# Performance work log

Measured on AMD Instinct MI355X. Metric: run time of the kernel, lower is better.

Reference implementation:

```python
import jax, jax.numpy as jnp
import numpy as np

B, S, D, H = 4, 4096, 1024, 64

def setup_inputs() -> dict:
    key = jax.random.key(0)
    k1, k2, k3, k4 = jax.random.split(key, 4)
    x = jax.random.normal(k1, (B, S, D), dtype=jnp.float32)
    scale = D ** -0.5
    Wq = jax.random.normal(k2, (D, H), dtype=jnp.float32) * scale
    Wk = jax.random.normal(k3, (D, H), dtype=jnp.float32) * scale
    Wv = jax.random.normal(k4, (D, H), dtype=jnp.float32) * scale
    return {"x": x, "Wq": Wq, "Wk": Wk, "Wv": Wv}

def reference(x, Wq, Wk, Wv):
    # Projections: [B,S,D] @ [D,H] -> [B,S,H]
    Q = jnp.einsum('bsd,dh->bsh', x, Wq)
    K = jnp.einsum('bsd,dh->bsh', x, Wk)
    V = jnp.einsum('bsd,dh->bsh', x, Wv)
    H_ = Q.shape[-1]
    # Scores [B,S,S], scaled by head_size**-0.5
    scores = jnp.einsum('bqh,bkh->bqk', Q, K) * (H_ ** -0.5)
    attn = jax.nn.softmax(scores, axis=-1)
    return jnp.einsum('bqk,bkh->bqh', attn, V)
```

## Files before the change

kernel.cpp:

```cpp
#include <hip/hip_runtime.h>
#include <hip/hip_bf16.h>

#define B_ 4
#define S_ 4096
#define D_ 1024
#define H_ 64

typedef __attribute__((ext_vector_type(8))) short bf16x8;
typedef __attribute__((ext_vector_type(4))) float f32x4;

static __device__ __forceinline__ unsigned short f2bf(float f) {
    union { float f; unsigned int i; } v; v.f = f;
    unsigned int r = v.i + 0x7FFFu + ((v.i >> 16) & 1u);
    return (unsigned short)(r >> 16);
}

static __device__ __forceinline__ float exp2_raw(float x) {
    return __builtin_amdgcn_exp2f(x);
}

typedef __attribute__((address_space(3))) unsigned int lds_u32;
typedef __attribute__((address_space(1))) const unsigned int glb_u32;
static __device__ __forceinline__ void gload16(const void* g, void* l) {
    __builtin_amdgcn_global_load_lds((glb_u32*)g, (lds_u32*)l, 16, 0, 0);
}

__global__ __launch_bounds__(256) void prep_w(
    const float* __restrict__ Wq, const float* __restrict__ Wk,
    const float* __restrict__ Wv, unsigned short* __restrict__ WF)
{
    __shared__ float wt[256][64];
    const int bid = blockIdx.x;
    const int y = bid >> 2, kr = (bid & 3) * 256;
    const float* W = (y == 0) ? Wq : (y == 1) ? Wk : Wv;
    const float scale = (y == 0) ? 0.125f * 1.4426950408889634f : 1.0f;
    const int t = threadIdx.x;

    #pragma unroll
    for (int it = 0; it < 16; ++it) {
        int idx = it * 256 + t;
        int k = idx >> 4, h4 = (idx & 15) * 4;
        *(float4*)&wt[k][h4] = *(const float4*)(W + (size_t)(kr + k) * H_ + h4);
    }
    __syncthreads();

    const int ntl = t >> 6, l = t & 63, lm = l & 15, lg = l >> 4;
    const int h = ntl * 16 + lm;
    #pragma unroll
    for (int g = 0; g < 8; ++g) {
        bf16x8 v;
        #pragma unroll
        for (int e = 0; e < 8; ++e) v[e] = f2bf(wt[g * 32 + lg * 8 + e][h] * scale);
        int ntg = y * 4 + ntl, gg = (kr >> 5) + g;
        *(bf16x8*)(WF + ((size_t)(ntg * 32 + gg) * 64 + l) * 8) = v;
    }
}

__global__ __launch_bounds__(512) void proj_mfma(
    const float* __restrict__ x, const unsigned short* __restrict__ WF,
    unsigned short* __restrict__ Qw, unsigned short* __restrict__ Kw,
    unsigned short* __restrict__ Vtw)
{
    __shared__ __align__(16) char pool[65536];

    const int tid = threadIdx.x;
    const int w = tid >> 6, l = tid & 63;
    const int lm = l & 15, lg = l >> 4;
    const int wm = w >> 2, wn = w & 3;
    const int row0 = blockIdx.x * 64;

    f32x4 acc[2][3];
    #pragma unroll
    for (int mt = 0; mt < 2; ++mt)
        #pragma unroll
        for (int n = 0; n < 3; ++n) acc[mt][n] = (f32x4){0.f, 0.f, 0.f, 0.f};

    auto stage = [&](int t) {
        #pragma unroll
        for (int j = 0; j < 2; ++j) {
            int i = (w * 2 + j) * 64 + l;
            int row = i >> 4;
            int u = ((i & 15) << 4) ^ ((row & 7) << 4);
            const char* g = (const char*)x + ((size_t)(row0 + row) << 12) + (t << 8) + u;
            char* dst = pool + (t & 3) * 16384 + ((w * 2 + j) << 10);
            gload16(g, dst);
        }
    };

    auto loadB = [&](int t, bf16x8* bf) {
        #pragma unroll
        for (int n = 0; n < 3; ++n)
            #pragma unroll
            for (int gg = 0; gg < 2; ++gg)
                bf[n * 2 + gg] = *(const bf16x8*)(WF +
                    ((size_t)((wn * 3 + n) * 32 + (t * 2 + gg)) * 64 + l) * 8);
    };

    auto compute = [&](int t, const bf16x8* bf) {
        const char* base = pool + (t & 3) * 16384;
        #pragma unroll
        for (int gg = 0; gg < 2; ++gg) {
            bf16x8 af[2];
            #pragma unroll
            for (int mt = 0; mt < 2; ++mt) {
                int r = wm * 32 + mt * 16 + lm;
                int sw = (r & 7) << 4;
                int c0 = gg * 128 + lg * 32;
                f32x4 a0 = *(const f32x4*)(base + r * 256 + (c0 ^ sw));
                f32x4 a1 = *(const f32x4*)(base + r * 256 + ((c0 + 16) ^ sw));
                af[mt][0] = f2bf(a0[0]); af[mt][1] = f2bf(a0[1]);
                af[mt][2] = f2bf(a0[2]); af[mt][3] = f2bf(a0[3]);
                af[mt][4] = f2bf(a1[0]); af[mt][5] = f2bf(a1[1]);
                af[mt][6] = f2bf(a1[2]); af[mt][7] = f2bf(a1[3]);
            }
            #pragma unroll
            for (int mt = 0; mt < 2; ++mt)
                #pragma unroll
                for (int n = 0; n < 3; ++n)
                    acc[mt][n] = __builtin_amdgcn_mfma_f32_16x16x32_bf16(
                        af[mt], bf[n * 2 + gg], acc[mt][n], 0, 0, 0);
        }
    };

    bf16x8 bA[6], bB[6];
    stage(0); stage(1); loadB(0, bA);

    #pragma unroll
    for (int tt = 0; tt < 16; tt += 2) {
        if (tt + 2 < 16) stage(tt + 2);
        loadB(tt + 1, bB);
        if (tt < 14) { asm volatile("s_waitcnt vmcnt(8)" ::: "memory"); }
        else         { asm volatile("s_waitcnt vmcnt(6)" ::: "memory"); }
        __builtin_amdgcn_sched_barrier(0);
        __builtin_amdgcn_s_barrier();
        __builtin_amdgcn_sched_barrier(0);
        compute(tt, bA);

        if (tt + 3 < 16) stage(tt + 3);
        if (tt + 2 < 16) loadB(tt + 2, bA);
        if (tt + 2 < 16) { asm volatile("s_waitcnt vmcnt(8)" ::: "memory"); }
        else             { asm volatile("s_waitcnt vmcnt(0)" ::: "memory"); }
        __builtin_amdgcn_sched_barrier(0);
        __builtin_amdgcn_s_barrier();
        __builtin_amdgcn_sched_barrier(0);
        compute(tt + 1, bB);
    }

    __syncthreads();
    unsigned short* et = (unsigned short*)pool;
    #pragma unroll
    for (int mt = 0; mt < 2; ++mt)
        #pragma unroll
        for (int n = 0; n < 3; ++n)
            #pragma unroll
            for (int reg = 0; reg < 4; ++reg)
                et[(wm * 32 + mt * 16 + lg * 4 + reg) * 200 + (wn * 48 + n * 16 + lm)] =
                    f2bf(acc[mt][n][reg]);
    __syncthreads();

    #pragma unroll
    for (int p = 0; p < 2; ++p) {
        int r = tid >> 3;
        int c = ((tid & 7) + p * 8) * 8;
        bf16x8 v = *(const bf16x8*)(et + r * 200 + c);
        unsigned short* dst = (c < 64) ? Qw : Kw;
        *(bf16x8*)(dst + (size_t)(row0 + r) * H_ + (c & 63)) = v;
    }
    {
        int h = tid & 63, i0 = (tid >> 6) * 8;
        bf16x8 v;
        #pragma unroll
        for (int i = 0; i < 8; ++i) v[i] = et[(i0 + i) * 200 + 128 + h];
        int bat = row0 >> 12, s0 = (row0 & (S_ - 1)) + i0;
        *(bf16x8*)(Vtw + ((size_t)bat * H_ + h) * S_ + s0) = v;
    }
}

__global__ __launch_bounds__(256, 4) void attn_kernel(
    const unsigned short* __restrict__ Qg, const unsigned short* __restrict__ Kg,
    const unsigned short* __restrict__ Vtg,
    float* __restrict__ Op, float2* __restrict__ Ml, int chunk)
{
    __shared__ __align__(16) char kv_lds[2][16384];
    __shared__ __align__(16) unsigned short pt[4][1024];

    const int tid = threadIdx.x;
    const int l = tid & 63, w = tid >> 6;
    const int lm = l & 15, lg = l >> 4;
    const int b = blockIdx.y, z = blockIdx.z;
    const int q0 = blockIdx.x * 64;
    const int kvbase = z * chunk;
    const int ntile = chunk >> 6;

    bf16x8 qa[2];
    {
        const unsigned short* qp =
            Qg + ((size_t)(b * S_ + q0 + w * 16 + lm)) * H_ + lg * 8;
        qa[0] = *(const bf16x8*)qp;
        qa[1] = *(const bf16x8*)(qp + 32);
    }

    f32x4 oa[4];
    float lsum = 0.f;
    #pragma unroll
    for (int nt = 0; nt < 4; ++nt) oa[nt] = (f32x4){0.f, 0.f, 0.f, 0.f};
    unsigned short* ptw = pt[w];

    const char* Kb = (const char*)Kg + ((size_t)b * S_ + kvbase) * (H_ * 2);
    const char* Vb = (const char*)Vtg + ((size_t)b * H_) * (S_ * 2) + (size_t)kvbase * 2;

    auto stage = [&](int t, int buf) {
        #pragma unroll
        for (int j = 0; j < 2; ++j) {
            int slot = w * 2 + j;
            int row = slot * 8 + (l >> 3), c16 = l & 7;
            int u = (c16 * 16) ^ ((row & 7) << 4);
            gload16(Kb + (size_t)(t * 64 + row) * 128 + u,
                    &kv_lds[buf][slot * 1024]);
            gload16(Vb + (size_t)row * (S_ * 2) + t * 128 + u,
                    &kv_lds[buf][8192 + slot * 1024]);
        }
    };

    stage(0, 0);
    asm volatile("s_waitcnt vmcnt(0)" ::: "memory");
    __builtin_amdgcn_s_barrier();

    for (int t = 0; t < ntile; ++t) {
        const int cur = t & 1;
        if (t + 1 < ntile) stage(t + 1, cur ^ 1);

        const char* kbase = kv_lds[cur];
        const char* vbase = kv_lds[cur] + 8192;

        f32x4 sv[4];
        __builtin_amdgcn_s_setprio(1);
        #pragma unroll
        for (int nt = 0; nt < 4; ++nt) {
            int r = nt * 16 + lm, sw = (r & 7) << 4;
            bf16x8 kb0 = *(const bf16x8*)(kbase + r * 128 + ((lg * 16) ^ sw));
            bf16x8 kb1 = *(const bf16x8*)(kbase + r * 128 + ((64 + lg * 16) ^ sw));
            f32x4 a = (f32x4){0.f, 0.f, 0.f, 0.f};
            a = __builtin_amdgcn_mfma_f32_16x16x32_bf16(kb0, qa[0], a, 0, 0, 0);
            a = __builtin_amdgcn_mfma_f32_16x16x32_bf16(kb1, qa[1], a, 0, 0, 0);
            sv[nt] = a;
        }
        __builtin_amdgcn_s_setprio(0);

        float p[4][4];
        float rs = 0.f;
        #pragma unroll
        for (int nt = 0; nt < 4; ++nt)
            #pragma unroll
            for (int reg = 0; reg < 4; ++reg) {
                p[nt][reg] = exp2_raw(sv[nt][reg]);
                rs += p[nt][reg];
            }
        lsum += rs;

        #pragma unroll
        for (int nt = 0; nt < 4; ++nt) {
            uint2 pv;
            asm("v_cvt_pk_bf16_f32 %0, %1, %2"
                : "=v"(pv.x) : "v"(p[nt][0]), "v"(p[nt][1]));
            asm("v_cvt_pk_bf16_f32 %0, %1, %2"
                : "=v"(pv.y) : "v"(p[nt][2]), "v"(p[nt][3]));
            *(uint2*)((char*)ptw + lm * 128 +
                      ((nt * 32 + lg * 8) ^ ((lm & 7) << 4))) = pv;
        }
        asm volatile("s_waitcnt lgkmcnt(0)" ::: "memory");
        __builtin_amdgcn_sched_barrier(0);

        __builtin_amdgcn_s_setprio(1);
        #pragma unroll
        for (int kk = 0; kk < 2; ++kk) {
            bf16x8 pb = *(const bf16x8*)((const char*)ptw + lm * 128 +
                                         ((kk * 64 + lg * 16) ^ ((lm & 7) << 4)));
            #pragma unroll
            for (int nt = 0; nt < 4; ++nt) {
                int hr = nt * 16 + lm, sw = (hr & 7) << 4;
                bf16x8 vb = *(const bf16x8*)(vbase + hr * 128 +
                                             ((kk * 64 + lg * 16) ^ sw));
                oa[nt] = __builtin_amdgcn_mfma_f32_16x16x32_bf16(
                    vb, pb, oa[nt], 0, 0, 0);
            }
        }
        __builtin_amdgcn_s_setprio(0);

        asm volatile("s_waitcnt vmcnt(0)" ::: "memory");
        __builtin_amdgcn_sched_barrier(0);
        __builtin_amdgcn_s_barrier();
        __builtin_amdgcn_sched_barrier(0);
    }

    const size_t zb = (size_t)z * B_ + b;

    {
        float rs = lsum;
        rs += __shfl_xor(rs, 16);
        rs += __shfl_xor(rs, 32);
        if (lg == 0) {
            const size_t qrow = zb * S_ + q0 + w * 16 + lm;
            Ml[qrow] = make_float2(0.f, rs);
        }
    }

    __syncthreads();
    {
        char* ot = kv_lds[0] + w * 8192;
        #pragma unroll
        for (int nt = 0; nt < 4; ++nt) {
            int off = ((nt * 16 + lg * 4) * 4) ^ ((lm & 7) << 4);
            *(f32x4*)(ot + lm * 256 + off) = oa[nt];
        }
        asm volatile("s_waitcnt lgkmcnt(0)" ::: "memory");
        __builtin_amdgcn_sched_barrier(0);
        int q = l >> 2;
        const size_t qrow = zb * S_ + q0 + w * 16 + q;
        #pragma unroll
        for (int i = 0; i < 4; ++i) {
            int h = (l & 3) * 4 + i * 16;
            f32x4 v = *(const f32x4*)(ot + q * 256 + (((h * 4)) ^ ((q & 7) << 4)));
            *(f32x4*)(Op + qrow * H_ + h) = v;
        }
    }
}

__global__ __launch_bounds__(256) void combine_kernel(
    const float* __restrict__ Op, const float2* __restrict__ Ml,
    float* __restrict__ out, int nsplit)
{
    const int idx = blockIdx.x * 256 + threadIdx.x;
    const int bq = idx >> 4;
    const int h4 = (idx & 15) * 4;
    const size_t BS = (size_t)B_ * S_;

    float M = -INFINITY;
    for (int i = 0; i < nsplit; ++i) M = fmaxf(M, Ml[i * BS + bq].x);
    float L = 0.f;
    float4 acc = make_float4(0.f, 0.f, 0.f, 0.f);
    for (int i = 0; i < nsplit; ++i) {
        float2 ml = Ml[i * BS + bq];
        float wgt = __builtin_amdgcn_exp2f(ml.x - M);
        L += wgt * ml.y;
        float4 o = *(const float4*)(Op + (i * BS + bq) * H_ + h4);
        acc.x += wgt * o.x; acc.y += wgt * o.y; acc.z += wgt * o.z; acc.w += wgt * o.w;
    }
    float inv = 1.f / L;
    float4 r = make_float4(acc.x * inv, acc.y * inv, acc.z * inv, acc.w * inv);
    *(float4*)(out + (size_t)bq * H_ + h4) = r;
}

extern "C" void kernel_launch(void* const* d_in, const int* in_sizes, int n_in,
                              void* d_out, int out_size, void* d_ws, size_t ws_size,
                              hipStream_t stream) {
    const float* x  = (const float*)d_in[0];
    const float* Wq = (const float*)d_in[1];
    const float* Wk = (const float*)d_in[2];
    const float* Wv = (const float*)d_in[3];

    const size_t NQ = (size_t)B_ * S_ * H_;
    unsigned short* Qw  = (unsigned short*)d_ws;
    unsigned short* Kw  = Qw + NQ;
    unsigned short* Vtw = Kw + NQ;
    unsigned short* WFw = Vtw + NQ;
    char* p = (char*)(WFw + 192 * D_);

    const size_t per_split = NQ * 4 + (size_t)B_ * S_ * 8;
    size_t used = 3 * NQ * 2 + 192 * D_ * 2;
    int nsplit = 4;
    while (nsplit > 1 && used + (size_t)nsplit * per_split > ws_size) nsplit >>= 1;

    float*  Op = (float*)p;
    float2* Ml = (float2*)(p + (size_t)nsplit * NQ * 4);
    float* out = (float*)d_out;

    prep_w<<<12, 256, 0, stream>>>(Wq, Wk, Wv, WFw);

    proj_mfma<<<B_ * S_ / 64, 512, 0, stream>>>(x, WFw, Qw, Kw, Vtw);

    dim3 agrid(S_ / 64, B_, nsplit);
    attn_kernel<<<agrid, 256, 0, stream>>>(Qw, Kw, Vtw, Op, Ml, S_ / nsplit);

    dim3 cgrid(B_ * S_ * 16 / 256);
    combine_kernel<<<cgrid, 256, 0, stream>>>(Op, Ml, out, nsplit);
}
```

Baseline: 60.31 us.

## Feed P directly from registers into 16x16x16 MFMAs, dropping LDS round-trip

The softmax probabilities were written to a per-wave LDS tile and read back as the PV MFMA operand. They are now kept in registers and consumed by 16x16x16 bf16 MFMAs, whose B-operand layout matches the S accumulator layout. This removes the LDS store, the wait and the reload. V fragments are loaded as 4-element vectors, which doubles the number of MFMA issues for PV. Launch bounds occupancy rises to 5 and the KV split count rises from 4 to 8, which adds more partial outputs for the combine kernel to merge.

```diff
diff --git a/kernel.cpp b/kernel.cpp
--- a/kernel.cpp
+++ b/kernel.cpp
@@ -7,6 +7,7 @@
 #define H_ 64
 
 typedef __attribute__((ext_vector_type(8))) short bf16x8;
+typedef __attribute__((ext_vector_type(4))) short bf16x4;
 typedef __attribute__((ext_vector_type(4))) float f32x4;
 
 static __device__ __forceinline__ unsigned short f2bf(float f) {
@@ -176,13 +177,12 @@
     }
 }
 
-__global__ __launch_bounds__(256, 4) void attn_kernel(
+__global__ __launch_bounds__(256, 5) void attn_kernel(
     const unsigned short* __restrict__ Qg, const unsigned short* __restrict__ Kg,
     const unsigned short* __restrict__ Vtg,
     float* __restrict__ Op, float2* __restrict__ Ml, int chunk)
 {
     __shared__ __align__(16) char kv_lds[2][16384];
-    __shared__ __align__(16) unsigned short pt[4][1024];
 
     const int tid = threadIdx.x;
     const int l = tid & 63, w = tid >> 6;
@@ -204,7 +204,6 @@
     float lsum = 0.f;
     #pragma unroll
     for (int nt = 0; nt < 4; ++nt) oa[nt] = (f32x4){0.f, 0.f, 0.f, 0.f};
-    unsigned short* ptw = pt[w];
 
     const char* Kb = (const char*)Kg + ((size_t)b * S_ + kvbase) * (H_ * 2);
     const char* Vb = (const char*)Vtg + ((size_t)b * H_) * (S_ * 2) + (size_t)kvbase * 2;
@@ -247,6 +246,16 @@
         }
         __builtin_amdgcn_s_setprio(0);
 
+        bf16x4 vf[4][4];
+        #pragma unroll
+        for (int ht = 0; ht < 4; ++ht) {
+            int hr = ht * 16 + lm, sw = (hr & 7) << 4;
+            #pragma unroll
+            for (int nt = 0; nt < 4; ++nt)
+                vf[ht][nt] = *(const bf16x4*)(vbase + hr * 128 +
+                                              ((nt * 32 + lg * 8) ^ sw));
+        }
+
         float p[4][4];
         float rs = 0.f;
         #pragma unroll
@@ -258,33 +267,24 @@
             }
         lsum += rs;
 
+        bf16x4 pf[4];
         #pragma unroll
         for (int nt = 0; nt < 4; ++nt) {
-            uint2 pv;
+            union { unsigned int u[2]; bf16x4 v; } pk;
             asm("v_cvt_pk_bf16_f32 %0, %1, %2"
-                : "=v"(pv.x) : "v"(p[nt][0]), "v"(p[nt][1]));
+                : "=v"(pk.u[0]) : "v"(p[nt][0]), "v"(p[nt][1]));
             asm("v_cvt_pk_bf16_f32 %0, %1, %2"
-                : "=v"(pv.y) : "v"(p[nt][2]), "v"(p[nt][3]));
-            *(uint2*)((char*)ptw + lm * 128 +
-                      ((nt * 32 + lg * 8) ^ ((lm & 7) << 4))) = pv;
-        }
-        asm volatile("s_waitcnt lgkmcnt(0)" ::: "memory");
-        __builtin_amdgcn_sched_barrier(0);
+                : "=v"(pk.u[1]) : "v"(p[nt][2]), "v"(p[nt][3]));
+            pf[nt] = pk.v;
+        }
 
         __builtin_amdgcn_s_setprio(1);
         #pragma unroll
-        for (int kk = 0; kk < 2; ++kk) {
-            bf16x8 pb = *(const bf16x8*)((const char*)ptw + lm * 128 +
-                                         ((kk * 64 + lg * 16) ^ ((lm & 7) << 4)));
-            #pragma unroll
-            for (int nt = 0; nt < 4; ++nt) {
-                int hr = nt * 16 + lm, sw = (hr & 7) << 4;
-                bf16x8 vb = *(const bf16x8*)(vbase + hr * 128 +
-                                             ((kk * 64 + lg * 16) ^ sw));
-                oa[nt] = __builtin_amdgcn_mfma_f32_16x16x32_bf16(
-                    vb, pb, oa[nt], 0, 0, 0);
-            }
-        }
+        for (int nt = 0; nt < 4; ++nt)
+            #pragma unroll
+            for (int ht = 0; ht < 4; ++ht)
+                oa[ht] = __builtin_amdgcn_mfma_f32_16x16x16bf16_1k(
+                    vf[ht][nt], pf[nt], oa[ht], 0, 0, 0);
         __builtin_amdgcn_s_setprio(0);
 
         asm volatile("s_waitcnt vmcnt(0)" ::: "memory");
@@ -368,7 +368,7 @@
 
     const size_t per_split = NQ * 4 + (size_t)B_ * S_ * 8;
     size_t used = 3 * NQ * 2 + 192 * D_ * 2;
-    int nsplit = 4;
+    int nsplit = 8;
     while (nsplit > 1 && used + (size_t)nsplit * per_split > ws_size) nsplit >>= 1;
 
     float*  Op = (float*)p;
```

New measurement: 65.28 us. +8.2%, slower.
